# Optimization experiments

Measured on AMD Instinct MI355X. Metric: run time of the kernel, lower is better.

## Reference

```python
import jax, jax.numpy as jnp
import numpy as np

C_MID = 32  # inChannels // 8
# Packing order matches torch loop: diagonal offset -i for i in 0..C-1,
# i.e. pairs (j+i, j) for j in 0..C-1-i, concatenated.
_ROWS = np.concatenate([np.arange(C_MID - i) + i for i in range(C_MID)])
_COLS = np.concatenate([np.arange(C_MID - i) for i in range(C_MID)])


def _bn_relu(y, g, b, m, v, eps=1e-5):
    # y: (B, C, H, W); per-channel affine BN (eval-style) + relu
    inv = g / jnp.sqrt(v + eps)
    return jax.nn.relu(y * inv[:, None, None] + (b - m * inv)[:, None, None])


def setup_inputs() -> dict:
    key = jax.random.key(0)
    ks = jax.random.split(key, 14)
    B, Cin, H, W = 16, 256, 64, 64
    mid, T, Cout = C_MID, C_MID * (C_MID + 1) // 2, 256
    return {
        "x": jax.random.normal(ks[0], (B, Cin, H, W), jnp.float32),
        "w1": jax.random.normal(ks[1], (mid, Cin), jnp.float32) * 0.05,
        "b1": jax.random.normal(ks[2], (mid,), jnp.float32) * 0.05,
        "g1": jax.random.uniform(ks[3], (mid,), jnp.float32, 0.5, 1.5),
        "be1": jax.random.normal(ks[4], (mid,), jnp.float32) * 0.1,
        "m1": jax.random.normal(ks[5], (mid,), jnp.float32) * 0.1,
        "v1": jax.random.uniform(ks[6], (mid,), jnp.float32, 0.5, 1.5),
        "w2": jax.random.normal(ks[7], (Cout, T), jnp.float32) * 0.05,
        "b2": jax.random.normal(ks[8], (Cout,), jnp.float32) * 0.05,
        "g2": jax.random.uniform(ks[9], (Cout,), jnp.float32, 0.5, 1.5),
        "be2": jax.random.normal(ks[10], (Cout,), jnp.float32) * 0.1,
        "m2": jax.random.normal(ks[11], (Cout,), jnp.float32) * 0.1,
        "v2": jax.random.uniform(ks[12], (Cout,), jnp.float32, 0.5, 1.5),
    }


def reference(x, w1, b1, g1, be1, m1, v1, w2, b2, g2, be2, m2, v2):
    # dimReduceLayer1: 1x1 conv + BN + relu
    y = jnp.einsum('bchw,oc->bohw', x, w1) + b1[:, None, None]
    y = _bn_relu(y, g1, be1, m1, v1)                       # (B, mid, H, W)
    yb = jnp.transpose(y, (0, 2, 3, 1))                    # (B, H, W, mid)
    rows = jnp.asarray(_ROWS)
    cols = jnp.asarray(_COLS)
    # Packed lower-triangular bilinear features, exactly the torch diagonal+cat order.
    packed = yb[..., rows] * yb[..., cols]                 # (B, H, W, T)
    # dimReduceLayer2: 1x1 conv + BN + relu
    z = jnp.einsum('bhwt,ot->bohw', packed, w2) + b2[:, None, None]
    return _bn_relu(z, g2, be2, m2, v2)
```

## Files before the change

### kernel.cpp

```cpp
#include <hip/hip_runtime.h>

#define EPS 1e-5f

typedef float f32x4 __attribute__((ext_vector_type(4)));
typedef short bf16x8 __attribute__((ext_vector_type(8)));

__device__ __forceinline__ unsigned short f2bf(float f) {
  unsigned int u = __builtin_bit_cast(unsigned int, f);
  u = (u + 0x7FFFu + ((u >> 16) & 1u)) >> 16;
  return (unsigned short)u;
}

__global__ __launch_bounds__(256) void k_prep(
    const float* __restrict__ w1, const float* __restrict__ b1,
    const float* __restrict__ g1, const float* __restrict__ be1,
    const float* __restrict__ m1, const float* __restrict__ v1,
    const float* __restrict__ w2, const float* __restrict__ b2,
    const float* __restrict__ g2, const float* __restrict__ be2,
    const float* __restrict__ m2, const float* __restrict__ v2,
    float* __restrict__ beta1, float* __restrict__ beta2,
    unsigned short* __restrict__ w1b, unsigned short* __restrict__ w2f)
{
  int t = blockIdx.x * 256 + threadIdx.x;
  if (t < 139264) {
    int j = t & 7, l = (t >> 3) & 63, g = t >> 9;
    int ct = g & 15, ks = g >> 4;
    int k = ks * 32 + (l >> 4) * 8 + j;
    int ch = ct * 16 + (l & 15);
    float val = 0.f;
    if (k < 528) {
      float s2 = g2[ch] * rsqrtf(v2[ch] + EPS);
      val = w2[ch * 528 + k] * s2;
    }
    w2f[t] = f2bf(val);
  }
  if (t < 8192) {
    int j = t & 7, l = (t >> 3) & 63, g = t >> 9;
    int ct = g & 1, ks = g >> 1;
    int c = ks * 32 + (l >> 4) * 8 + j;
    int m = ct * 16 + (l & 15);
    float s1 = g1[m] * rsqrtf(v1[m] + EPS);
    w1b[t] = f2bf(w1[m * 256 + c] * s1);
  }
  if (t < 32) {
    float s1 = g1[t] * rsqrtf(v1[t] + EPS);
    beta1[t] = (b1[t] - m1[t]) * s1 + be1[t];
  }
  if (t < 256) {
    float s2 = g2[t] * rsqrtf(v2[t] + EPS);
    beta2[t] = (b2[t] - m2[t]) * s2 + be2[t];
  }
}

template<int I>
__device__ __forceinline__ void do_diag(const float* __restrict__ y,
                                        unsigned short* __restrict__ pr)
{
  constexpr int L = 32 - I;
  constexpr int base = 32 * I - (I * (I - 1)) / 2;
  float p[L];
#pragma unroll
  for (int j = 0; j < L; ++j) p[j] = y[I + j] * y[j];
  constexpr int s = (base & 1) ? 1 : 0;
  if constexpr (s != 0) pr[base] = f2bf(p[0]);
#pragma unroll
  for (int j = s; j + 1 < L; j += 2)
    *(unsigned int*)&pr[base + j] =
        (unsigned int)f2bf(p[j]) | ((unsigned int)f2bf(p[j + 1]) << 16);
  if constexpr (((L - s) & 1) != 0) pr[base + L - 1] = f2bf(p[L - 1]);
}

template<int S>
__device__ __forceinline__ void do_set(const float* __restrict__ y,
                                       unsigned short* __restrict__ pr)
{
  do_diag<S>(y, pr);
  do_diag<31 - S>(y, pr);
  do_diag<S + 8>(y, pr);
  do_diag<23 - S>(y, pr);
}

__global__ __launch_bounds__(256, 4) void k_fused(
    const float* __restrict__ x, const unsigned short* __restrict__ w1b,
    const float* __restrict__ beta1, const unsigned short* __restrict__ w2f,
    const float* __restrict__ beta2, float* __restrict__ out)
{
  __shared__ __align__(16) unsigned short pk[32 * 548];
  __shared__ __align__(8) float yf[32 * 34];
  int tid = threadIdx.x;
  int wv = tid >> 6, lane = tid & 63;
  int l15 = lane & 15, l4 = lane >> 4;
  int g = blockIdx.x;
  int orig = ((g & 7) << 8) + (g >> 3);
  int pb = orig * 32;
  int b = pb >> 12, hw0 = pb & 4095;
  const float* xb = x + ((size_t)b << 20) + hw0;

  unsigned short* xt = pk;
  {
    int q = tid & 7;
    int cg = tid >> 3;
#pragma unroll
    for (int pass = 0; pass < 2; ++pass) {
      int c4 = cg + pass * 32;
      float4 v[4];
#pragma unroll
      for (int i = 0; i < 4; ++i)
        v[i] = *(const float4*)&xb[(size_t)(4 * c4 + i) * 4096 + 4 * q];
#pragma unroll
      for (int s = 0; s < 4; ++s) {
        float e0 = ((const float*)&v[0])[s];
        float e1 = ((const float*)&v[1])[s];
        float e2 = ((const float*)&v[2])[s];
        float e3 = ((const float*)&v[3])[s];
        unsigned int lo = (unsigned int)f2bf(e0) | ((unsigned int)f2bf(e1) << 16);
        unsigned int hi = (unsigned int)f2bf(e2) | ((unsigned int)f2bf(e3) << 16);
        *(uint2*)&xt[(4 * q + s) * 276 + 4 * c4] = make_uint2(lo, hi);
      }
    }
  }
  __syncthreads();

  {
    int pxt = wv & 1, mt = wv >> 1;
    int px = pxt * 16 + l15;
    f32x4 acc1 = (f32x4){0.f, 0.f, 0.f, 0.f};
    const uint4* w1b4 = (const uint4*)w1b;
#pragma unroll
    for (int ks = 0; ks < 8; ++ks) {
      union { uint4 q; bf16x8 v; } A, B;
      A.q = w1b4[(ks * 2 + mt) * 64 + lane];
      const unsigned short* s = &xt[px * 276 + ks * 32 + l4 * 8];
      uint2 lo = *(const uint2*)s;
      uint2 hi = *(const uint2*)(s + 4);
      B.q = make_uint4(lo.x, lo.y, hi.x, hi.y);
      acc1 = __builtin_amdgcn_mfma_f32_16x16x32_bf16(A.v, B.v, acc1, 0, 0, 0);
    }
    int m0 = mt * 16 + l4 * 4;
#pragma unroll
    for (int r = 0; r < 4; ++r)
      yf[px * 34 + m0 + r] = fmaxf(acc1[r] + beta1[m0 + r], 0.f);
  }
  __syncthreads();

  {
    int px2 = tid & 31, set = tid >> 5;
    const float* yr = &yf[px2 * 34];
    unsigned short* pr = &pk[px2 * 548];
    float y[32];
#pragma unroll
    for (int k = 0; k < 16; ++k) {
      float2 v = *(const float2*)&yr[2 * k];
      y[2 * k] = v.x; y[2 * k + 1] = v.y;
    }
    switch (set) {
      case 0: do_set<0>(y, pr); break;
      case 1: do_set<1>(y, pr); break;
      case 2: do_set<2>(y, pr); break;
      case 3: do_set<3>(y, pr); break;
      case 4: do_set<4>(y, pr); break;
      case 5: do_set<5>(y, pr); break;
      case 6: do_set<6>(y, pr); break;
      default: do_set<7>(y, pr); break;
    }
    if (set < 4) {
      *(unsigned int*)&pr[528 + set * 4] = 0u;
      *(unsigned int*)&pr[530 + set * 4] = 0u;
    }
  }

  float bet[4][4];
#pragma unroll
  for (int ctl = 0; ctl < 4; ++ctl)
#pragma unroll
    for (int r = 0; r < 4; ++r)
      bet[ctl][r] = beta2[(wv * 4 + ctl) * 16 + l4 * 4 + r];

  __syncthreads();

  f32x4 acc[2][4];
#pragma unroll
  for (int a = 0; a < 2; ++a)
#pragma unroll
    for (int c = 0; c < 4; ++c)
      acc[a][c] = (f32x4){0.f, 0.f, 0.f, 0.f};

  const uint4* w2f4 = (const uint4*)w2f;
#pragma unroll
  for (int ks = 0; ks < 17; ++ks) {
    union { uint4 q; bf16x8 v; } A[4], B[2];
#pragma unroll
    for (int ctl = 0; ctl < 4; ++ctl)
      A[ctl].q = w2f4[(ks * 16 + wv * 4 + ctl) * 64 + lane];
#pragma unroll
    for (int pt = 0; pt < 2; ++pt) {
      const unsigned short* src = &pk[(pt * 16 + l15) * 548 + ks * 32 + l4 * 8];
      uint2 lo = *(const uint2*)src;
      uint2 hi = *(const uint2*)(src + 4);
      B[pt].q = make_uint4(lo.x, lo.y, hi.x, hi.y);
    }
#pragma unroll
    for (int pt = 0; pt < 2; ++pt)
#pragma unroll
      for (int ctl = 0; ctl < 4; ++ctl)
        acc[pt][ctl] = __builtin_amdgcn_mfma_f32_16x16x32_bf16(
            A[ctl].v, B[pt].v, acc[pt][ctl], 0, 0, 0);
  }

#pragma unroll
  for (int pt = 0; pt < 2; ++pt) {
    int hw = hw0 + pt * 16 + l15;
#pragma unroll
    for (int ctl = 0; ctl < 4; ++ctl) {
      int ch = (wv * 4 + ctl) * 16 + l4 * 4;
#pragma unroll
      for (int r = 0; r < 4; ++r) {
        float v = fmaxf(acc[pt][ctl][r] + bet[ctl][r], 0.f);
        out[(((size_t)b * 256 + (ch + r)) << 12) + hw] = v;
      }
    }
  }
}

extern "C" void kernel_launch(void* const* d_in, const int* in_sizes, int n_in,
                              void* d_out, int out_size, void* d_ws, size_t ws_size,
                              hipStream_t stream)
{
  const float* x   = (const float*)d_in[0];
  const float* w1  = (const float*)d_in[1];
  const float* b1  = (const float*)d_in[2];
  const float* g1  = (const float*)d_in[3];
  const float* be1 = (const float*)d_in[4];
  const float* m1  = (const float*)d_in[5];
  const float* v1  = (const float*)d_in[6];
  const float* w2  = (const float*)d_in[7];
  const float* b2  = (const float*)d_in[8];
  const float* g2  = (const float*)d_in[9];
  const float* be2 = (const float*)d_in[10];
  const float* m2  = (const float*)d_in[11];
  const float* v2  = (const float*)d_in[12];

  char* ws = (char*)d_ws;
  float*          beta1 = (float*)(ws);
  float*          beta2 = (float*)(ws + 128);
  unsigned short* w1b   = (unsigned short*)(ws + 1152);
  unsigned short* w2f   = (unsigned short*)(ws + 17536);
  float* out = (float*)d_out;

  k_prep<<<dim3(544), dim3(256), 0, stream>>>(
      w1, b1, g1, be1, m1, v1, w2, b2, g2, be2, m2, v2, beta1, beta2, w1b, w2f);
  k_fused<<<dim3(2048), dim3(256), 0, stream>>>(x, w1b, beta1, w2f, beta2, out);
}
```

Measured before the change: 48.60 us.

## Process two tiles per block with register prefetch of next x tile

Halves the grid so each block processes two 32-pixel tiles. The x loads for the second tile are issued into registers right after the first tile's transpose, so they overlap the first tile's GEMMs. Float-to-bf16 packing now uses the hardware v_cvt_pk_bf16_f32 instruction instead of manual rounding. The block-index swizzle is dropped, and holding 8 float4 in registers raises register pressure, which may reduce occupancy or latency hiding.

```diff
diff --git a/kernel.cpp b/kernel.cpp
--- a/kernel.cpp
+++ b/kernel.cpp
@@ -9,6 +9,12 @@
   unsigned int u = __builtin_bit_cast(unsigned int, f);
   u = (u + 0x7FFFu + ((u >> 16) & 1u)) >> 16;
   return (unsigned short)u;
+}
+
+__device__ __forceinline__ unsigned int cvt2(float a, float b) {
+  unsigned int r;
+  asm("v_cvt_pk_bf16_f32 %0, %1, %2" : "=v"(r) : "v"(a), "v"(b));
+  return r;
 }
 
 __global__ __launch_bounds__(256) void k_prep(
@@ -65,8 +71,7 @@
   if constexpr (s != 0) pr[base] = f2bf(p[0]);
 #pragma unroll
   for (int j = s; j + 1 < L; j += 2)
-    *(unsigned int*)&pr[base + j] =
-        (unsigned int)f2bf(p[j]) | ((unsigned int)f2bf(p[j + 1]) << 16);
+    *(unsigned int*)&pr[base + j] = cvt2(p[j], p[j + 1]);
   if constexpr (((L - s) & 1) != 0) pr[base + L - 1] = f2bf(p[L - 1]);
 }
 
@@ -91,132 +96,152 @@
   int wv = tid >> 6, lane = tid & 63;
   int l15 = lane & 15, l4 = lane >> 4;
   int g = blockIdx.x;
-  int orig = ((g & 7) << 8) + (g >> 3);
-  int pb = orig * 32;
-  int b = pb >> 12, hw0 = pb & 4095;
-  const float* xb = x + ((size_t)b << 20) + hw0;
-
-  unsigned short* xt = pk;
+  int q = tid & 7;
+  int cg = tid >> 3;
+
+  float4 xr[8];
   {
-    int q = tid & 7;
-    int cg = tid >> 3;
+    int pb = g * 32;
+    const float* xb = x + ((size_t)(pb >> 12) << 20) + (pb & 4095);
+#pragma unroll
+    for (int pass = 0; pass < 2; ++pass)
+#pragma unroll
+      for (int i = 0; i < 4; ++i)
+        xr[pass * 4 + i] =
+            *(const float4*)&xb[(size_t)(4 * (cg + pass * 32) + i) * 4096 + 4 * q];
+  }
+
+  for (int t = 0; t < 2; ++t) {
+    int tile = g + t * 1024;
+    int pb = tile * 32;
+    int b = pb >> 12, hw0 = pb & 4095;
+
+    if (t) __syncthreads();
+
+    unsigned short* xt = pk;
 #pragma unroll
     for (int pass = 0; pass < 2; ++pass) {
       int c4 = cg + pass * 32;
-      float4 v[4];
-#pragma unroll
-      for (int i = 0; i < 4; ++i)
-        v[i] = *(const float4*)&xb[(size_t)(4 * c4 + i) * 4096 + 4 * q];
 #pragma unroll
       for (int s = 0; s < 4; ++s) {
-        float e0 = ((const float*)&v[0])[s];
-        float e1 = ((const float*)&v[1])[s];
-        float e2 = ((const float*)&v[2])[s];
-        float e3 = ((const float*)&v[3])[s];
-        unsigned int lo = (unsigned int)f2bf(e0) | ((unsigned int)f2bf(e1) << 16);
-        unsigned int hi = (unsigned int)f2bf(e2) | ((unsigned int)f2bf(e3) << 16);
-        *(uint2*)&xt[(4 * q + s) * 276 + 4 * c4] = make_uint2(lo, hi);
-      }
-    }
-  }
-  __syncthreads();
-
-  {
-    int pxt = wv & 1, mt = wv >> 1;
-    int px = pxt * 16 + l15;
-    f32x4 acc1 = (f32x4){0.f, 0.f, 0.f, 0.f};
-    const uint4* w1b4 = (const uint4*)w1b;
-#pragma unroll
-    for (int ks = 0; ks < 8; ++ks) {
-      union { uint4 q; bf16x8 v; } A, B;
-      A.q = w1b4[(ks * 2 + mt) * 64 + lane];
-      const unsigned short* s = &xt[px * 276 + ks * 32 + l4 * 8];
-      uint2 lo = *(const uint2*)s;
-      uint2 hi = *(const uint2*)(s + 4);
-      B.q = make_uint4(lo.x, lo.y, hi.x, hi.y);
-      acc1 = __builtin_amdgcn_mfma_f32_16x16x32_bf16(A.v, B.v, acc1, 0, 0, 0);
-    }
-    int m0 = mt * 16 + l4 * 4;
-#pragma unroll
-    for (int r = 0; r < 4; ++r)
-      yf[px * 34 + m0 + r] = fmaxf(acc1[r] + beta1[m0 + r], 0.f);
-  }
-  __syncthreads();
-
-  {
-    int px2 = tid & 31, set = tid >> 5;
-    const float* yr = &yf[px2 * 34];
-    unsigned short* pr = &pk[px2 * 548];
-    float y[32];
-#pragma unroll
-    for (int k = 0; k < 16; ++k) {
-      float2 v = *(const float2*)&yr[2 * k];
-      y[2 * k] = v.x; y[2 * k + 1] = v.y;
-    }
-    switch (set) {
-      case 0: do_set<0>(y, pr); break;
-      case 1: do_set<1>(y, pr); break;
-      case 2: do_set<2>(y, pr); break;
-      case 3: do_set<3>(y, pr); break;
-      case 4: do_set<4>(y, pr); break;
-      case 5: do_set<5>(y, pr); break;
-      case 6: do_set<6>(y, pr); break;
-      default: do_set<7>(y, pr); break;
-    }
-    if (set < 4) {
-      *(unsigned int*)&pr[528 + set * 4] = 0u;
-      *(unsigned int*)&pr[530 + set * 4] = 0u;
-    }
-  }
-
-  float bet[4][4];
-#pragma unroll
-  for (int ctl = 0; ctl < 4; ++ctl)
-#pragma unroll
-    for (int r = 0; r < 4; ++r)
-      bet[ctl][r] = beta2[(wv * 4 + ctl) * 16 + l4 * 4 + r];
-
-  __syncthreads();
-
-  f32x4 acc[2][4];
-#pragma unroll
-  for (int a = 0; a < 2; ++a)
-#pragma unroll
-    for (int c = 0; c < 4; ++c)
-      acc[a][c] = (f32x4){0.f, 0.f, 0.f, 0.f};
-
-  const uint4* w2f4 = (const uint4*)w2f;
-#pragma unroll
-  for (int ks = 0; ks < 17; ++ks) {
-    union { uint4 q; bf16x8 v; } A[4], B[2];
+        const float* v0 = (const float*)&xr[pass * 4 + 0];
+        const float* v1 = (const float*)&xr[pass * 4 + 1];
+        const float* v2 = (const float*)&xr[pass * 4 + 2];
+        const float* v3 = (const float*)&xr[pass * 4 + 3];
+        *(uint2*)&xt[(4 * q + s) * 276 + 4 * c4] =
+            make_uint2(cvt2(v0[s], v1[s]), cvt2(v2[s], v3[s]));
+      }
+    }
+    __syncthreads();
+
+    if (t == 0) {
+      int pb1 = (g + 1024) * 32;
+      const float* xb1 = x + ((size_t)(pb1 >> 12) << 20) + (pb1 & 4095);
+#pragma unroll
+      for (int pass = 0; pass < 2; ++pass)
+#pragma unroll
+        for (int i = 0; i < 4; ++i)
+          xr[pass * 4 + i] =
+              *(const float4*)&xb1[(size_t)(4 * (cg + pass * 32) + i) * 4096 + 4 * q];
+    }
+
+    {
+      int pxt = wv & 1, mt = wv >> 1;
+      int px = pxt * 16 + l15;
+      f32x4 acc1 = (f32x4){0.f, 0.f, 0.f, 0.f};
+      const uint4* w1b4 = (const uint4*)w1b;
+#pragma unroll
+      for (int ks = 0; ks < 8; ++ks) {
+        union { uint4 q; bf16x8 v; } A, B;
+        A.q = w1b4[(ks * 2 + mt) * 64 + lane];
+        const unsigned short* s = &xt[px * 276 + ks * 32 + l4 * 8];
+        uint2 lo = *(const uint2*)s;
+        uint2 hi = *(const uint2*)(s + 4);
+        B.q = make_uint4(lo.x, lo.y, hi.x, hi.y);
+        acc1 = __builtin_amdgcn_mfma_f32_16x16x32_bf16(A.v, B.v, acc1, 0, 0, 0);
+      }
+      int m0 = mt * 16 + l4 * 4;
+#pragma unroll
+      for (int r = 0; r < 4; ++r)
+        yf[px * 34 + m0 + r] = fmaxf(acc1[r] + beta1[m0 + r], 0.f);
+    }
+    __syncthreads();
+
+    {
+      int px2 = tid & 31, set = tid >> 5;
+      const float* yr = &yf[px2 * 34];
+      unsigned short* pr = &pk[px2 * 548];
+      float y[32];
+#pragma unroll
+      for (int k = 0; k < 16; ++k) {
+        float2 v = *(const float2*)&yr[2 * k];
+        y[2 * k] = v.x; y[2 * k + 1] = v.y;
+      }
+      switch (set) {
+        case 0: do_set<0>(y, pr); break;
+        case 1: do_set<1>(y, pr); break;
+        case 2: do_set<2>(y, pr); break;
+        case 3: do_set<3>(y, pr); break;
+        case 4: do_set<4>(y, pr); break;
+        case 5: do_set<5>(y, pr); break;
+        case 6: do_set<6>(y, pr); break;
+        default: do_set<7>(y, pr); break;
+      }
+      if (set < 4) {
+        *(unsigned int*)&pr[528 + set * 4] = 0u;
+        *(unsigned int*)&pr[530 + set * 4] = 0u;
+      }
+    }
+
+    float bet[4][4];
 #pragma unroll
     for (int ctl = 0; ctl < 4; ++ctl)
-      A[ctl].q = w2f4[(ks * 16 + wv * 4 + ctl) * 64 + lane];
+#pragma unroll
+      for (int r = 0; r < 4; ++r)
+        bet[ctl][r] = beta2[(wv * 4 + ctl) * 16 + l4 * 4 + r];
+
+    __syncthreads();
+
+    f32x4 acc[2][4];
+#pragma unroll
+    for (int a = 0; a < 2; ++a)
+#pragma unroll
+      for (int c = 0; c < 4; ++c)
+        acc[a][c] = (f32x4){0.f, 0.f, 0.f, 0.f};
+
+    const uint4* w2f4 = (const uint4*)w2f;
+#pragma unroll
+    for (int ks = 0; ks < 17; ++ks) {
+      union { uint4 q; bf16x8 v; } A[4], B[2];
+#pragma unroll
+      for (int ctl = 0; ctl < 4; ++ctl)
+        A[ctl].q = w2f4[(ks * 16 + wv * 4 + ctl) * 64 + lane];
+#pragma unroll
+      for (int pt = 0; pt < 2; ++pt) {
+        const unsigned short* src = &pk[(pt * 16 + l15) * 548 + ks * 32 + l4 * 8];
+        uint2 lo = *(const uint2*)src;
+        uint2 hi = *(const uint2*)(src + 4);
+        B[pt].q = make_uint4(lo.x, lo.y, hi.x, hi.y);
+      }
+#pragma unroll
+      for (int pt = 0; pt < 2; ++pt)
+#pragma unroll
+        for (int ctl = 0; ctl < 4; ++ctl)
+          acc[pt][ctl] = __builtin_amdgcn_mfma_f32_16x16x32_bf16(
+              A[ctl].v, B[pt].v, acc[pt][ctl], 0, 0, 0);
+    }
+
 #pragma unroll
     for (int pt = 0; pt < 2; ++pt) {
-      const unsigned short* src = &pk[(pt * 16 + l15) * 548 + ks * 32 + l4 * 8];
-      uint2 lo = *(const uint2*)src;
-      uint2 hi = *(const uint2*)(src + 4);
-      B[pt].q = make_uint4(lo.x, lo.y, hi.x, hi.y);
-    }
-#pragma unroll
-    for (int pt = 0; pt < 2; ++pt)
-#pragma unroll
-      for (int ctl = 0; ctl < 4; ++ctl)
-        acc[pt][ctl] = __builtin_amdgcn_mfma_f32_16x16x32_bf16(
-            A[ctl].v, B[pt].v, acc[pt][ctl], 0, 0, 0);
-  }
-
-#pragma unroll
-  for (int pt = 0; pt < 2; ++pt) {
-    int hw = hw0 + pt * 16 + l15;
-#pragma unroll
-    for (int ctl = 0; ctl < 4; ++ctl) {
-      int ch = (wv * 4 + ctl) * 16 + l4 * 4;
-#pragma unroll
-      for (int r = 0; r < 4; ++r) {
-        float v = fmaxf(acc[pt][ctl][r] + bet[ctl][r], 0.f);
-        out[(((size_t)b * 256 + (ch + r)) << 12) + hw] = v;
+      int hw = hw0 + pt * 16 + l15;
+#pragma unroll
+      for (int ctl = 0; ctl < 4; ++ctl) {
+        int ch = (wv * 4 + ctl) * 16 + l4 * 4;
+#pragma unroll
+        for (int r = 0; r < 4; ++r) {
+          float v = fmaxf(acc[pt][ctl][r] + bet[ctl][r], 0.f);
+          out[(((size_t)b * 256 + (ch + r)) << 12) + hw] = v;
+        }
       }
     }
   }
@@ -249,5 +274,5 @@
 
   k_prep<<<dim3(544), dim3(256), 0, stream>>>(
       w1, b1, g1, be1, m1, v1, w2, b2, g2, be2, m2, v2, beta1, beta2, w1b, w2f);
-  k_fused<<<dim3(2048), dim3(256), 0, stream>>>(x, w1b, beta1, w2f, beta2, out);
-}
+  k_fused<<<dim3(1024), dim3(256), 0, stream>>>(x, w1b, beta1, w2f, beta2, out);
+}
```

After: 173.4 us. 257% more time.

## Double pixel tile per block to 64 and use packed bf16 conversion

Applied to the files above, without the earlier changes.

Each block now handles 64 pixels instead of 32, so every w2 A-fragment loaded from global memory feeds twice as many MFMAs, halving weight traffic per output. The first GEMM now has each wave compute both 16-channel tiles for its own 16 pixels. Manual f32-to-bf16 rounding is replaced with the v_cvt_pk_bf16_f32 instruction. In exchange, LDS use doubles to about 78KB, the occupancy hint is dropped and the accumulators grow to 64 floats per lane, which lowers occupancy and halves the grid to 1024 blocks; the ks loop is also no longer unrolled.

```diff
diff --git a/kernel.cpp b/kernel.cpp
--- a/kernel.cpp
+++ b/kernel.cpp
@@ -9,6 +9,12 @@
   unsigned int u = __builtin_bit_cast(unsigned int, f);
   u = (u + 0x7FFFu + ((u >> 16) & 1u)) >> 16;
   return (unsigned short)u;
+}
+
+__device__ __forceinline__ unsigned int cvt2(float a, float b) {
+  unsigned int r;
+  asm("v_cvt_pk_bf16_f32 %0, %1, %2" : "=v"(r) : "v"(a), "v"(b));
+  return r;
 }
 
 __global__ __launch_bounds__(256) void k_prep(
@@ -65,8 +71,7 @@
   if constexpr (s != 0) pr[base] = f2bf(p[0]);
 #pragma unroll
   for (int j = s; j + 1 < L; j += 2)
-    *(unsigned int*)&pr[base + j] =
-        (unsigned int)f2bf(p[j]) | ((unsigned int)f2bf(p[j + 1]) << 16);
+    *(unsigned int*)&pr[base + j] = cvt2(p[j], p[j + 1]);
   if constexpr (((L - s) & 1) != 0) pr[base + L - 1] = f2bf(p[L - 1]);
 }
 
@@ -80,94 +85,105 @@
   do_diag<23 - S>(y, pr);
 }
 
-__global__ __launch_bounds__(256, 4) void k_fused(
+__device__ __forceinline__ void p2_half(const float* __restrict__ yfh,
+                                        unsigned short* __restrict__ pkh,
+                                        int tid)
+{
+  int px2 = tid & 31, set = tid >> 5;
+  const float* yr = &yfh[px2 * 34];
+  unsigned short* pr = &pkh[px2 * 548];
+  float y[32];
+#pragma unroll
+  for (int k = 0; k < 16; ++k) {
+    float2 v = *(const float2*)&yr[2 * k];
+    y[2 * k] = v.x; y[2 * k + 1] = v.y;
+  }
+  switch (set) {
+    case 0: do_set<0>(y, pr); break;
+    case 1: do_set<1>(y, pr); break;
+    case 2: do_set<2>(y, pr); break;
+    case 3: do_set<3>(y, pr); break;
+    case 4: do_set<4>(y, pr); break;
+    case 5: do_set<5>(y, pr); break;
+    case 6: do_set<6>(y, pr); break;
+    default: do_set<7>(y, pr); break;
+  }
+  if (set < 4) {
+    *(unsigned int*)&pr[528 + set * 4] = 0u;
+    *(unsigned int*)&pr[530 + set * 4] = 0u;
+  }
+}
+
+__global__ __launch_bounds__(256) void k_fused(
     const float* __restrict__ x, const unsigned short* __restrict__ w1b,
     const float* __restrict__ beta1, const unsigned short* __restrict__ w2f,
     const float* __restrict__ beta2, float* __restrict__ out)
 {
-  __shared__ __align__(16) unsigned short pk[32 * 548];
-  __shared__ __align__(8) float yf[32 * 34];
+  __shared__ __align__(16) unsigned short pk[64 * 548];
+  __shared__ __align__(8) float yf[64 * 34];
   int tid = threadIdx.x;
   int wv = tid >> 6, lane = tid & 63;
   int l15 = lane & 15, l4 = lane >> 4;
   int g = blockIdx.x;
-  int orig = ((g & 7) << 8) + (g >> 3);
-  int pb = orig * 32;
+  int orig = ((g & 7) << 7) + (g >> 3);
+  int pb = orig * 64;
   int b = pb >> 12, hw0 = pb & 4095;
   const float* xb = x + ((size_t)b << 20) + hw0;
 
   unsigned short* xt = pk;
   {
-    int q = tid & 7;
-    int cg = tid >> 3;
-#pragma unroll
-    for (int pass = 0; pass < 2; ++pass) {
-      int c4 = cg + pass * 32;
+    int q = tid & 15;
+    int c40 = tid >> 4;
+#pragma unroll
+    for (int pass = 0; pass < 4; ++pass) {
+      int c4 = c40 + pass * 16;
       float4 v[4];
 #pragma unroll
       for (int i = 0; i < 4; ++i)
         v[i] = *(const float4*)&xb[(size_t)(4 * c4 + i) * 4096 + 4 * q];
 #pragma unroll
       for (int s = 0; s < 4; ++s) {
-        float e0 = ((const float*)&v[0])[s];
-        float e1 = ((const float*)&v[1])[s];
-        float e2 = ((const float*)&v[2])[s];
-        float e3 = ((const float*)&v[3])[s];
-        unsigned int lo = (unsigned int)f2bf(e0) | ((unsigned int)f2bf(e1) << 16);
-        unsigned int hi = (unsigned int)f2bf(e2) | ((unsigned int)f2bf(e3) << 16);
-        *(uint2*)&xt[(4 * q + s) * 276 + 4 * c4] = make_uint2(lo, hi);
+        const float* e0 = (const float*)&v[0];
+        const float* e1 = (const float*)&v[1];
+        const float* e2 = (const float*)&v[2];
+        const float* e3 = (const float*)&v[3];
+        *(uint2*)&xt[(4 * q + s) * 276 + 4 * c4] =
+            make_uint2(cvt2(e0[s], e1[s]), cvt2(e2[s], e3[s]));
       }
     }
   }
   __syncthreads();
 
   {
-    int pxt = wv & 1, mt = wv >> 1;
-    int px = pxt * 16 + l15;
-    f32x4 acc1 = (f32x4){0.f, 0.f, 0.f, 0.f};
+    int px = wv * 16 + l15;
+    f32x4 acc1[2];
+    acc1[0] = (f32x4){0.f, 0.f, 0.f, 0.f};
+    acc1[1] = (f32x4){0.f, 0.f, 0.f, 0.f};
     const uint4* w1b4 = (const uint4*)w1b;
 #pragma unroll
     for (int ks = 0; ks < 8; ++ks) {
-      union { uint4 q; bf16x8 v; } A, B;
-      A.q = w1b4[(ks * 2 + mt) * 64 + lane];
+      union { uint4 q; bf16x8 v; } A0, A1, B;
+      A0.q = w1b4[(ks * 2 + 0) * 64 + lane];
+      A1.q = w1b4[(ks * 2 + 1) * 64 + lane];
       const unsigned short* s = &xt[px * 276 + ks * 32 + l4 * 8];
       uint2 lo = *(const uint2*)s;
       uint2 hi = *(const uint2*)(s + 4);
       B.q = make_uint4(lo.x, lo.y, hi.x, hi.y);
-      acc1 = __builtin_amdgcn_mfma_f32_16x16x32_bf16(A.v, B.v, acc1, 0, 0, 0);
-    }
-    int m0 = mt * 16 + l4 * 4;
-#pragma unroll
-    for (int r = 0; r < 4; ++r)
-      yf[px * 34 + m0 + r] = fmaxf(acc1[r] + beta1[m0 + r], 0.f);
+      acc1[0] = __builtin_amdgcn_mfma_f32_16x16x32_bf16(A0.v, B.v, acc1[0], 0, 0, 0);
+      acc1[1] = __builtin_amdgcn_mfma_f32_16x16x32_bf16(A1.v, B.v, acc1[1], 0, 0, 0);
+    }
+#pragma unroll
+    for (int ct = 0; ct < 2; ++ct) {
+      int m0 = ct * 16 + l4 * 4;
+#pragma unroll
+      for (int r = 0; r < 4; ++r)
+        yf[px * 34 + m0 + r] = fmaxf(acc1[ct][r] + beta1[m0 + r], 0.f);
+    }
   }
   __syncthreads();
 
-  {
-    int px2 = tid & 31, set = tid >> 5;
-    const float* yr = &yf[px2 * 34];
-    unsigned short* pr = &pk[px2 * 548];
-    float y[32];
-#pragma unroll
-    for (int k = 0; k < 16; ++k) {
-      float2 v = *(const float2*)&yr[2 * k];
-      y[2 * k] = v.x; y[2 * k + 1] = v.y;
-    }
-    switch (set) {
-      case 0: do_set<0>(y, pr); break;
-      case 1: do_set<1>(y, pr); break;
-      case 2: do_set<2>(y, pr); break;
-      case 3: do_set<3>(y, pr); break;
-      case 4: do_set<4>(y, pr); break;
-      case 5: do_set<5>(y, pr); break;
-      case 6: do_set<6>(y, pr); break;
-      default: do_set<7>(y, pr); break;
-    }
-    if (set < 4) {
-      *(unsigned int*)&pr[528 + set * 4] = 0u;
-      *(unsigned int*)&pr[530 + set * 4] = 0u;
-    }
-  }
+  p2_half(yf, pk, tid);
+  p2_half(yf + 32 * 34, pk + 32 * 548, tid);
 
   float bet[4][4];
 #pragma unroll
@@ -178,29 +194,28 @@
 
   __syncthreads();
 
-  f32x4 acc[2][4];
-#pragma unroll
-  for (int a = 0; a < 2; ++a)
+  f32x4 acc[4][4];
+#pragma unroll
+  for (int a = 0; a < 4; ++a)
 #pragma unroll
     for (int c = 0; c < 4; ++c)
       acc[a][c] = (f32x4){0.f, 0.f, 0.f, 0.f};
 
   const uint4* w2f4 = (const uint4*)w2f;
-#pragma unroll
   for (int ks = 0; ks < 17; ++ks) {
-    union { uint4 q; bf16x8 v; } A[4], B[2];
+    union { uint4 q; bf16x8 v; } A[4], B[4];
 #pragma unroll
     for (int ctl = 0; ctl < 4; ++ctl)
       A[ctl].q = w2f4[(ks * 16 + wv * 4 + ctl) * 64 + lane];
 #pragma unroll
-    for (int pt = 0; pt < 2; ++pt) {
+    for (int pt = 0; pt < 4; ++pt) {
       const unsigned short* src = &pk[(pt * 16 + l15) * 548 + ks * 32 + l4 * 8];
       uint2 lo = *(const uint2*)src;
       uint2 hi = *(const uint2*)(src + 4);
       B[pt].q = make_uint4(lo.x, lo.y, hi.x, hi.y);
     }
 #pragma unroll
-    for (int pt = 0; pt < 2; ++pt)
+    for (int pt = 0; pt < 4; ++pt)
 #pragma unroll
       for (int ctl = 0; ctl < 4; ++ctl)
         acc[pt][ctl] = __builtin_amdgcn_mfma_f32_16x16x32_bf16(
@@ -208,7 +223,7 @@
   }
 
 #pragma unroll
-  for (int pt = 0; pt < 2; ++pt) {
+  for (int pt = 0; pt < 4; ++pt) {
     int hw = hw0 + pt * 16 + l15;
 #pragma unroll
     for (int ctl = 0; ctl < 4; ++ctl) {
@@ -249,5 +264,5 @@
 
   k_prep<<<dim3(544), dim3(256), 0, stream>>>(
       w1, b1, g1, be1, m1, v1, w2, b2, g2, be2, m2, v2, beta1, beta2, w1b, w2f);
-  k_fused<<<dim3(2048), dim3(256), 0, stream>>>(x, w1b, beta1, w2f, beta2, out);
-}
+  k_fused<<<dim3(1024), dim3(256), 0, stream>>>(x, w1b, beta1, w2f, beta2, out);
+}
```

After: 50.71 us. 1.04x slower.

## Split layer-1 conv into separate fp32 FMA kernel writing bf16 workspace

Applied to the files above, without the earlier changes.

Unfuses the first 1x1 conv from the main kernel. A new kernel computes it per pixel with scalar fp32 FMAs over all 256 channels and writes bf16 activations to a workspace. The second kernel then reads those activations instead of transposing x and running MFMA. Packed bf16 conversion now uses the v_cvt_pk_bf16_f32 instruction. This adds an extra launch and a global round trip. The new layer-1 kernel runs only 64-thread blocks and does its FMAs without tensor cores, which risks low throughput while it streams the 64 MB input.

```diff
diff --git a/kernel.cpp b/kernel.cpp
--- a/kernel.cpp
+++ b/kernel.cpp
@@ -9,6 +9,15 @@
   unsigned int u = __builtin_bit_cast(unsigned int, f);
   u = (u + 0x7FFFu + ((u >> 16) & 1u)) >> 16;
   return (unsigned short)u;
+}
+__device__ __forceinline__ float bf2f(unsigned short h) {
+  unsigned int u = ((unsigned int)h) << 16;
+  return __builtin_bit_cast(float, u);
+}
+__device__ __forceinline__ unsigned int cvt2(float a, float b) {
+  unsigned int r;
+  asm("v_cvt_pk_bf16_f32 %0, %1, %2" : "=v"(r) : "v"(a), "v"(b));
+  return r;
 }
 
 __global__ __launch_bounds__(256) void k_prep(
@@ -19,7 +28,7 @@
     const float* __restrict__ g2, const float* __restrict__ be2,
     const float* __restrict__ m2, const float* __restrict__ v2,
     float* __restrict__ beta1, float* __restrict__ beta2,
-    unsigned short* __restrict__ w1b, unsigned short* __restrict__ w2f)
+    float* __restrict__ w1f, unsigned short* __restrict__ w2f)
 {
   int t = blockIdx.x * 256 + threadIdx.x;
   if (t < 139264) {
@@ -35,12 +44,9 @@
     w2f[t] = f2bf(val);
   }
   if (t < 8192) {
-    int j = t & 7, l = (t >> 3) & 63, g = t >> 9;
-    int ct = g & 1, ks = g >> 1;
-    int c = ks * 32 + (l >> 4) * 8 + j;
-    int m = ct * 16 + (l & 15);
+    int c = t >> 5, m = t & 31;
     float s1 = g1[m] * rsqrtf(v1[m] + EPS);
-    w1b[t] = f2bf(w1[m * 256 + c] * s1);
+    w1f[t] = w1[m * 256 + c] * s1;
   }
   if (t < 32) {
     float s1 = g1[t] * rsqrtf(v1[t] + EPS);
@@ -52,6 +58,39 @@
   }
 }
 
+__global__ __launch_bounds__(64) void k_l1(
+    const float* __restrict__ x, const float* __restrict__ w1f,
+    const float* __restrict__ beta1, unsigned short* __restrict__ yws)
+{
+  int px = blockIdx.x * 64 + threadIdx.x;
+  int b = px >> 12, hw = px & 4095;
+  const float* xb = x + ((size_t)b << 20) + hw;
+
+  float acc[32];
+#pragma unroll
+  for (int m = 0; m < 32; ++m) acc[m] = 0.f;
+
+#pragma unroll 4
+  for (int c = 0; c < 256; ++c) {
+    float xv = xb[(size_t)c * 4096];
+    const float* wr = &w1f[c * 32];
+#pragma unroll
+    for (int m = 0; m < 32; ++m) acc[m] = fmaf(xv, wr[m], acc[m]);
+  }
+
+  unsigned int ow[16];
+#pragma unroll
+  for (int m = 0; m < 16; ++m) {
+    float a  = fmaxf(acc[2 * m]     + beta1[2 * m],     0.f);
+    float bv = fmaxf(acc[2 * m + 1] + beta1[2 * m + 1], 0.f);
+    ow[m] = cvt2(a, bv);
+  }
+  uint4* dst = (uint4*)(yws + (size_t)px * 32);
+#pragma unroll
+  for (int q = 0; q < 4; ++q)
+    dst[q] = make_uint4(ow[4 * q], ow[4 * q + 1], ow[4 * q + 2], ow[4 * q + 3]);
+}
+
 template<int I>
 __device__ __forceinline__ void do_diag(const float* __restrict__ y,
                                         unsigned short* __restrict__ pr)
@@ -65,8 +104,7 @@
   if constexpr (s != 0) pr[base] = f2bf(p[0]);
 #pragma unroll
   for (int j = s; j + 1 < L; j += 2)
-    *(unsigned int*)&pr[base + j] =
-        (unsigned int)f2bf(p[j]) | ((unsigned int)f2bf(p[j + 1]) << 16);
+    *(unsigned int*)&pr[base + j] = cvt2(p[j], p[j + 1]);
   if constexpr (((L - s) & 1) != 0) pr[base + L - 1] = f2bf(p[L - 1]);
 }
 
@@ -80,13 +118,11 @@
   do_diag<23 - S>(y, pr);
 }
 
-__global__ __launch_bounds__(256, 4) void k_fused(
-    const float* __restrict__ x, const unsigned short* __restrict__ w1b,
-    const float* __restrict__ beta1, const unsigned short* __restrict__ w2f,
+__global__ __launch_bounds__(256, 4) void k_l2(
+    const unsigned short* __restrict__ yws, const unsigned short* __restrict__ w2f,
     const float* __restrict__ beta2, float* __restrict__ out)
 {
   __shared__ __align__(16) unsigned short pk[32 * 548];
-  __shared__ __align__(8) float yf[32 * 34];
   int tid = threadIdx.x;
   int wv = tid >> 6, lane = tid & 63;
   int l15 = lane & 15, l4 = lane >> 4;
@@ -94,65 +130,22 @@
   int orig = ((g & 7) << 8) + (g >> 3);
   int pb = orig * 32;
   int b = pb >> 12, hw0 = pb & 4095;
-  const float* xb = x + ((size_t)b << 20) + hw0;
-
-  unsigned short* xt = pk;
-  {
-    int q = tid & 7;
-    int cg = tid >> 3;
-#pragma unroll
-    for (int pass = 0; pass < 2; ++pass) {
-      int c4 = cg + pass * 32;
-      float4 v[4];
-#pragma unroll
-      for (int i = 0; i < 4; ++i)
-        v[i] = *(const float4*)&xb[(size_t)(4 * c4 + i) * 4096 + 4 * q];
-#pragma unroll
-      for (int s = 0; s < 4; ++s) {
-        float e0 = ((const float*)&v[0])[s];
-        float e1 = ((const float*)&v[1])[s];
-        float e2 = ((const float*)&v[2])[s];
-        float e3 = ((const float*)&v[3])[s];
-        unsigned int lo = (unsigned int)f2bf(e0) | ((unsigned int)f2bf(e1) << 16);
-        unsigned int hi = (unsigned int)f2bf(e2) | ((unsigned int)f2bf(e3) << 16);
-        *(uint2*)&xt[(4 * q + s) * 276 + 4 * c4] = make_uint2(lo, hi);
-      }
-    }
-  }
-  __syncthreads();
-
-  {
-    int pxt = wv & 1, mt = wv >> 1;
-    int px = pxt * 16 + l15;
-    f32x4 acc1 = (f32x4){0.f, 0.f, 0.f, 0.f};
-    const uint4* w1b4 = (const uint4*)w1b;
-#pragma unroll
-    for (int ks = 0; ks < 8; ++ks) {
-      union { uint4 q; bf16x8 v; } A, B;
-      A.q = w1b4[(ks * 2 + mt) * 64 + lane];
-      const unsigned short* s = &xt[px * 276 + ks * 32 + l4 * 8];
-      uint2 lo = *(const uint2*)s;
-      uint2 hi = *(const uint2*)(s + 4);
-      B.q = make_uint4(lo.x, lo.y, hi.x, hi.y);
-      acc1 = __builtin_amdgcn_mfma_f32_16x16x32_bf16(A.v, B.v, acc1, 0, 0, 0);
-    }
-    int m0 = mt * 16 + l4 * 4;
-#pragma unroll
-    for (int r = 0; r < 4; ++r)
-      yf[px * 34 + m0 + r] = fmaxf(acc1[r] + beta1[m0 + r], 0.f);
-  }
-  __syncthreads();
 
   {
     int px2 = tid & 31, set = tid >> 5;
-    const float* yr = &yf[px2 * 34];
+    const uint4* y4 = (const uint4*)(yws + (size_t)(pb + px2) * 32);
+    float y[32];
+#pragma unroll
+    for (int qq = 0; qq < 4; ++qq) {
+      uint4 v = y4[qq];
+      unsigned int ua[4] = {v.x, v.y, v.z, v.w};
+#pragma unroll
+      for (int w = 0; w < 4; ++w) {
+        y[qq * 8 + 2 * w]     = bf2f((unsigned short)(ua[w] & 0xFFFFu));
+        y[qq * 8 + 2 * w + 1] = bf2f((unsigned short)(ua[w] >> 16));
+      }
+    }
     unsigned short* pr = &pk[px2 * 548];
-    float y[32];
-#pragma unroll
-    for (int k = 0; k < 16; ++k) {
-      float2 v = *(const float2*)&yr[2 * k];
-      y[2 * k] = v.x; y[2 * k + 1] = v.y;
-    }
     switch (set) {
       case 0: do_set<0>(y, pr); break;
       case 1: do_set<1>(y, pr); break;
@@ -243,11 +236,13 @@
   char* ws = (char*)d_ws;
   float*          beta1 = (float*)(ws);
   float*          beta2 = (float*)(ws + 128);
-  unsigned short* w1b   = (unsigned short*)(ws + 1152);
-  unsigned short* w2f   = (unsigned short*)(ws + 17536);
+  float*          w1f   = (float*)(ws + 1152);
+  unsigned short* w2f   = (unsigned short*)(ws + 33920);
+  unsigned short* yws   = (unsigned short*)(ws + 312448);
   float* out = (float*)d_out;
 
   k_prep<<<dim3(544), dim3(256), 0, stream>>>(
-      w1, b1, g1, be1, m1, v1, w2, b2, g2, be2, m2, v2, beta1, beta2, w1b, w2f);
-  k_fused<<<dim3(2048), dim3(256), 0, stream>>>(x, w1b, beta1, w2f, beta2, out);
-}
+      w1, b1, g1, be1, m1, v1, w2, b2, g2, be2, m2, v2, beta1, beta2, w1f, w2f);
+  k_l1<<<dim3(1024), dim3(64), 0, stream>>>(x, w1f, beta1, yws);
+  k_l2<<<dim3(2048), dim3(256), 0, stream>>>(yws, w2f, beta2, out);
+}
```

Measured after the change: 93.06 us. 1.91x slower.
